# Kernel tuning notes

Measured on AMD Instinct MI355X. Metric: run time of the kernel, lower is better.

The kernel has to match this reference:

```python
import jax, jax.numpy as jnp
import numpy as np

N_TREES = 512
DEPTH = 10
NODES_PER_TREE = 2 ** DEPTH - 1  # 1023, heap-indexed complete binary tree
N = N_TREES * NODES_PER_TREE     # 523776 nodes
X_SIZE = 128
H_SIZE = 128
NUM_CLASSES = 5
VOCAB = 32000


def _level_ids(l):
    """Global node ids for level l (root=0) and their child ids (None for leaves)."""
    start = 2 ** l - 1
    heap = start + np.arange(2 ** l)
    tree_off = np.arange(N_TREES)[:, None] * NODES_PER_TREE
    ids = (tree_off + heap[None, :]).reshape(-1)
    if l < DEPTH - 1:
        child_heap = np.stack([2 * heap + 1, 2 * heap + 2], axis=-1)  # [2^l, 2]
        child = (np.arange(N_TREES)[:, None, None] * NODES_PER_TREE
                 + child_heap[None]).reshape(-1, 2)
        return jnp.asarray(ids), jnp.asarray(child)
    return jnp.asarray(ids), None


def setup_inputs() -> dict:
    key = jax.random.key(0)
    ks = jax.random.split(key, 12)
    s = 0.05
    return {
        "wordid": jax.random.randint(ks[0], (N,), 0, VOCAB),
        "E":      jax.random.normal(ks[1], (VOCAB, X_SIZE), jnp.float32) * s,
        "W_iou":  jax.random.normal(ks[2], (3 * H_SIZE, X_SIZE), jnp.float32) * s,
        "b_iou":  jax.random.normal(ks[3], (3 * H_SIZE,), jnp.float32) * s,
        "U_iou":  jax.random.normal(ks[4], (3 * H_SIZE, H_SIZE), jnp.float32) * s,
        "b_Uiou": jax.random.normal(ks[5], (3 * H_SIZE,), jnp.float32) * s,
        "W_f":    jax.random.normal(ks[6], (H_SIZE, X_SIZE), jnp.float32) * s,
        "b_Wf":   jax.random.normal(ks[7], (H_SIZE,), jnp.float32) * s,
        "U_f":    jax.random.normal(ks[8], (H_SIZE, H_SIZE), jnp.float32) * s,
        "b_Uf":   jax.random.normal(ks[9], (H_SIZE,), jnp.float32) * s,
        "W_out":  jax.random.normal(ks[10], (NUM_CLASSES, H_SIZE), jnp.float32) * s,
        "b_out":  jax.random.normal(ks[11], (NUM_CLASSES,), jnp.float32) * s,
    }


def reference(wordid, E, W_iou, b_iou, U_iou, b_Uiou, W_f, b_Wf, U_f, b_Uf, W_out, b_out):
    mask = (wordid != -1)  # PAD_WORD mask; all-true for generated ids
    x = E[wordid * mask.astype(wordid.dtype)] * mask[:, None].astype(E.dtype)  # [N, X]

    h = jnp.zeros((N, H_SIZE), E.dtype)
    c = jnp.zeros((N, H_SIZE), E.dtype)

    # Topological traversal: leaves (deepest level) up to roots.
    for l in reversed(range(DEPTH)):
        ids, child = _level_ids(l)
        xl = x[ids]  # [M, X]
        if child is None:  # leaves: empty mailbox -> h_tild = c_tild = 0
            h_tild = jnp.zeros((ids.shape[0], H_SIZE), E.dtype)
            c_tild = h_tild
        else:
            hc = h[child]                               # mailbox h: [M, 2, H]
            cc = c[child]                               # mailbox c: [M, 2, H]
            h_tild = hc.sum(axis=1)                     # child-sum
            wx = xl @ W_f.T + b_Wf                      # [M, H]
            uh = hc @ U_f.T + b_Uf                      # [M, 2, H]
            f = jax.nn.sigmoid(wx[:, None, :] + uh)     # per-child forget gate
            c_tild = (f * cc).sum(axis=1)
        iou = xl @ W_iou.T + b_iou + h_tild @ U_iou.T + b_Uiou  # [M, 3H]
        i, o, u = jnp.split(iou, 3, axis=1)
        i, o, u = jax.nn.sigmoid(i), jax.nn.sigmoid(o), jnp.tanh(u)
        cl = i * u + c_tild
        hl = o * jnp.tanh(cl)
        h = h.at[ids].set(hl)
        c = c.at[ids].set(cl)

    # dropout is identity in eval / p=0.0
    logits = h @ W_out.T + b_out  # [N, num_classes]
    return logits
```

## Files before the change

### kernel.cpp

```cpp
#include <hip/hip_runtime.h>

#define H 128
#define TDEPTH 10
#define NPT 1023
#define NTREES 512

typedef unsigned short bf16_t;
typedef unsigned int u32;
typedef __attribute__((ext_vector_type(8))) short bf16x8;
typedef __attribute__((ext_vector_type(4))) float f32x4;

__device__ __forceinline__ float rcp_(float x) { return __builtin_amdgcn_rcpf(x); }
__device__ __forceinline__ float sig_(float x) { return rcp_(1.0f + __expf(-x)); }
__device__ __forceinline__ float th_(float x)  { return 1.0f - 2.0f * rcp_(__expf(2.0f * x) + 1.0f); }
__device__ __forceinline__ float b2f(u32 u) {
    union { float f; u32 u; } v; v.u = u << 16; return v.f;
}
__device__ __forceinline__ bf16_t f2b16(float f) {
    union { float f; u32 u; } v; v.f = f;
    return (bf16_t)((v.u + 0x7fffu + ((v.u >> 16) & 1u)) >> 16);
}
__device__ __forceinline__ bf16x8 ld8(const bf16_t* p) {
    return *reinterpret_cast<const bf16x8*>(p);
}
__device__ __forceinline__ bf16x8 ld8c(const char* p) {
    return *reinterpret_cast<const bf16x8*>(p);
}
__device__ __forceinline__ void gload16(const void* g, void* l) {
    __builtin_amdgcn_global_load_lds(
        (const __attribute__((address_space(1))) void*)g,
        (__attribute__((address_space(3))) void*)l, 16, 0, 0);
}
#define MFMA(a,b,c) __builtin_amdgcn_mfma_f32_16x16x32_bf16(a,b,c,0,0,0)

#define R_H  8192
#define R_C  24576
#define BUFSZ 40960

#define FX_SZ   24576
#define F_H     49152
#define F_C     65536
#define F_LDSSZ 81920

__global__ void pack_weights(const float* __restrict__ W_iou, const float* __restrict__ U_iou,
                             const float* __restrict__ W_f,   const float* __restrict__ U_f,
                             const float* __restrict__ W_out, bf16_t* __restrict__ Wb)
{
    int i = blockIdx.x * 256 + threadIdx.x;
    if (i < 131072) {
        int k    = i & 127;
        int p    = (i >> 7) & 7;
        int feat = i >> 10;
        float v;
        switch (p) {
            case 0: v = W_iou[(      feat) * H + k]; break;
            case 1: v = W_iou[(128 + feat) * H + k]; break;
            case 2: v = W_iou[(256 + feat) * H + k]; break;
            case 3: v = U_iou[(      feat) * H + k]; break;
            case 4: v = U_iou[(128 + feat) * H + k]; break;
            case 5: v = U_iou[(256 + feat) * H + k]; break;
            case 6: v = W_f  [feat * H + k]; break;
            default: v = U_f [feat * H + k]; break;
        }
        Wb[i] = f2b16(v);
    } else {
        int j = i - 131072;
        int cls = j >> 7, k = j & 127;
        Wb[i] = f2b16(cls < 5 ? W_out[cls * H + k] : 0.0f);
    }
}

__global__ void pack_E(const float* __restrict__ E, bf16_t* __restrict__ Eb)
{
    int i = blockIdx.x * 256 + threadIdx.x;
    Eb[i] = f2b16(E[i]);
}

__global__ __launch_bounds__(512, 2) void leaf8_fused(
    const int* __restrict__ wordid, const bf16_t* __restrict__ Eb,
    const bf16_t* __restrict__ Wb,
    const float* __restrict__ b_iou, const float* __restrict__ b_Uiou,
    const float* __restrict__ b_Wf,  const float* __restrict__ b_Uf,
    bf16_t* __restrict__ h_cur, bf16_t* __restrict__ c_cur,
    const float* __restrict__ b_out, float* __restrict__ out,
    int t0, int nt)
{
    extern __shared__ __align__(16) char lds_raw[];

    const int tid  = threadIdx.x;
    const int lane = tid & 63;
    const int w    = tid >> 6;
    const int l15  = lane & 15;
    const int kg   = lane >> 4;
    const int feat = w * 16 + l15;
    const int tilebase = blockIdx.x * nt;

    const float bi  = b_iou[      feat] + b_Uiou[      feat];
    const float bo  = b_iou[128 + feat] + b_Uiou[128 + feat];
    const float bu  = b_iou[256 + feat] + b_Uiou[256 + feat];
    const float bfv = b_Wf[feat] + b_Uf[feat];
    const f32x4 z = {0.f, 0.f, 0.f, 0.f};

    const bf16_t* wbase = Wb + (size_t)feat * 1024 + kg * 8;
    const bf16_t* Wob   = Wb + 131072;

    const int lrow = lane >> 4;
    const int colb = (lane & 15) * 16;

    struct Wids { int a, b, c; };
    auto loadwid = [&](int t) -> Wids {
        Wids r;
        int tb64 = (tilebase + t) * 64, tb32 = (tilebase + t) * 32;
        {   int gl = tb64 + w * 4 + lrow;
            int tt = gl >> 9, ii = gl & 511;
            r.a = wordid[(t0 + tt) * NPT + 511 + ii]; }
        {   int gl = tb64 + 32 + w * 4 + lrow;
            int tt = gl >> 9, ii = gl & 511;
            r.b = wordid[(t0 + tt) * NPT + 511 + ii]; }
        {   int gp = tb32 + w * 4 + lrow;
            int tt = gp >> 8, ii = gp & 255;
            r.c = wordid[(t0 + tt) * NPT + 255 + ii]; }
        return r;
    };

    auto issue = [&](const Wids& wd, char* xbuf) {
        {   int row = w * 4 + lrow;
            gload16((const char*)Eb + (size_t)wd.a * 256 + (colb ^ ((row & 7) << 4)),
                    xbuf + w * 1024); }
        {   int row = 32 + w * 4 + lrow;
            gload16((const char*)Eb + (size_t)wd.b * 256 + (colb ^ ((row & 7) << 4)),
                    xbuf + (w + 8) * 1024); }
        {   int row = w * 4 + lrow;
            gload16((const char*)Eb + (size_t)wd.c * 256 + (colb ^ ((row & 7) << 4)),
                    xbuf + (w + 16) * 1024); }
    };

    Wids wcur = loadwid(0);
    issue(wcur, lds_raw);
    if (nt > 1) wcur = loadwid(1);
    __syncthreads();

    char* h_s = lds_raw + F_H;
    char* c_s = lds_raw + F_C;

    for (int t = 0; t < nt; ++t) {
        char* xbuf  = lds_raw + (t & 1) * FX_SZ;
        char* xleaf = xbuf;
        char* xpar  = xbuf + 16384;
        const int n0 = (tilebase + t) * 32;

        f32x4 lac[3][4];
#pragma unroll
        for (int g = 0; g < 3; ++g)
#pragma unroll
            for (int m = 0; m < 4; ++m) lac[g][m] = z;

#pragma unroll
        for (int ks = 0; ks < 4; ++ks) {
            bf16x8 W0 = ld8(wbase + ks * 32 + 0 * 128);
            bf16x8 W1 = ld8(wbase + ks * 32 + 1 * 128);
            bf16x8 W2 = ld8(wbase + ks * 32 + 2 * 128);
            const int cb = (ks * 32 + kg * 8) * 2;
#pragma unroll
            for (int mt = 0; mt < 4; ++mt) {
                int row = mt * 16 + l15;
                bf16x8 xa = ld8c(xleaf + row * 256 + (cb ^ ((row & 7) << 4)));
                lac[0][mt] = MFMA(xa, W0, lac[0][mt]);
                lac[1][mt] = MFMA(xa, W1, lac[1][mt]);
                lac[2][mt] = MFMA(xa, W2, lac[2][mt]);
            }
        }

        if (t + 1 < nt) {
            issue(wcur, lds_raw + ((t + 1) & 1) * FX_SZ);
            if (t + 2 < nt) wcur = loadwid(t + 2);
        }

#pragma unroll
        for (int mt = 0; mt < 4; ++mt) {
#pragma unroll
            for (int r = 0; r < 4; ++r) {
                int j = mt * 16 + kg * 4 + r;
                float iv = sig_(lac[0][mt][r] + bi);
                float ov = sig_(lac[1][mt][r] + bo);
                float uv = th_ (lac[2][mt][r] + bu);
                float cl = iv * uv;
                float hl = ov * th_(cl);
                int off = j * 256 + ((feat * 2) ^ (((j >> 1) & 7) << 4));
                *(bf16_t*)(h_s + off) = f2b16(hl);
                *(bf16_t*)(c_s + off) = f2b16(cl);
            }
        }
        __syncthreads();

        f32x4 acc[6][2];
#pragma unroll
        for (int g = 0; g < 6; ++g)
#pragma unroll
            for (int m = 0; m < 2; ++m) acc[g][m] = z;

#pragma unroll
        for (int ks = 0; ks < 4; ++ks) {
            bf16x8 W0 = ld8(wbase + ks * 32 + 0 * 128);
            bf16x8 W1 = ld8(wbase + ks * 32 + 1 * 128);
            bf16x8 W2 = ld8(wbase + ks * 32 + 2 * 128);
            bf16x8 W3 = ld8(wbase + ks * 32 + 3 * 128);
            bf16x8 W4 = ld8(wbase + ks * 32 + 4 * 128);
            bf16x8 W5 = ld8(wbase + ks * 32 + 5 * 128);
            bf16x8 W6 = ld8(wbase + ks * 32 + 6 * 128);
            bf16x8 W7 = ld8(wbase + ks * 32 + 7 * 128);
            const int cb = (ks * 32 + kg * 8) * 2;
#pragma unroll
            for (int mt = 0; mt < 2; ++mt) {
                const int row = mt * 16 + l15;
                const int sw  = (row & 7) << 4;
                bf16x8 xa  = ld8c(xpar + row * 256 + (cb ^ sw));
                bf16x8 h0a = ld8c(h_s + (2 * row)     * 256 + (cb ^ sw));
                bf16x8 h1a = ld8c(h_s + (2 * row + 1) * 256 + (cb ^ sw));
                acc[0][mt] = MFMA(h1a, W3, MFMA(h0a, W3, MFMA(xa, W0, acc[0][mt])));
                acc[1][mt] = MFMA(h1a, W4, MFMA(h0a, W4, MFMA(xa, W1, acc[1][mt])));
                acc[2][mt] = MFMA(h1a, W5, MFMA(h0a, W5, MFMA(xa, W2, acc[2][mt])));
                acc[3][mt] = MFMA(xa,  W6, acc[3][mt]);
                acc[4][mt] = MFMA(h0a, W7, acc[4][mt]);
                acc[5][mt] = MFMA(h1a, W7, acc[5][mt]);
            }
        }

        if (w < 4) {
            const int pr = (w & 2) ? 1 : 0;
            const int mbase = (w & 1) * 16;
            f32x4 lacc = z;
#pragma unroll
            for (int ks = 0; ks < 4; ++ks) {
                const int cb = (ks * 32 + kg * 8) * 2;
                int prow = mbase + l15;
                bf16x8 ha = ld8c(h_s + (size_t)(2 * prow + pr) * 256
                                 + (cb ^ ((prow & 7) << 4)));
                bf16x8 wo = ld8(Wob + (size_t)l15 * 128 + ks * 32 + kg * 8);
                lacc = MFMA(ha, wo, lacc);
            }
            if (l15 < 5) {
                float bo5 = b_out[l15];
#pragma unroll
                for (int r = 0; r < 4; ++r) {
                    int m  = mbase + kg * 4 + r;
                    int gc = 2 * (n0 + m) + pr;
                    int tt = gc >> 9, ii = gc & 511;
                    out[(size_t)((t0 + tt) * NPT + 511 + ii) * 5 + l15] = lacc[r] + bo5;
                }
            }
        }

#pragma unroll
        for (int mt = 0; mt < 2; ++mt) {
#pragma unroll
            for (int r = 0; r < 4; ++r) {
                int nb = mt * 16 + kg * 4 + r;
                int g  = n0 + nb;
                float iv = sig_(acc[0][mt][r] + bi);
                float ov = sig_(acc[1][mt][r] + bo);
                float uv = th_ (acc[2][mt][r] + bu);
                float fx = acc[3][mt][r];
                float f0 = sig_(fx + acc[4][mt][r] + bfv);
                float f1 = sig_(fx + acc[5][mt][r] + bfv);
                int co = (feat * 2) ^ ((nb & 7) << 4);
                float c0 = b2f((u32)*(const bf16_t*)(c_s + (2 * nb)     * 256 + co));
                float c1 = b2f((u32)*(const bf16_t*)(c_s + (2 * nb + 1) * 256 + co));
                float cl = iv * uv + f0 * c0 + f1 * c1;
                float hl = ov * th_(cl);
                h_cur[(size_t)g * H + feat] = f2b16(hl);
                c_cur[(size_t)g * H + feat] = f2b16(cl);
            }
        }

        __syncthreads();
    }
}

__global__ __launch_bounds__(512, 2) void internal_mfma(
    const int* __restrict__ wordid, const bf16_t* __restrict__ Eb,
    const bf16_t* __restrict__ Wb,
    const float* __restrict__ b_iou, const float* __restrict__ b_Uiou,
    const float* __restrict__ b_Wf,  const float* __restrict__ b_Uf,
    const bf16_t* __restrict__ h_prev, const bf16_t* __restrict__ c_prev,
    bf16_t* __restrict__ h_cur, bf16_t* __restrict__ c_cur,
    const float* __restrict__ b_out, float* __restrict__ out,
    int level, int t0, int nt)
{
    extern __shared__ __align__(16) char lds_raw[];

    const int tid  = threadIdx.x;
    const int lane = tid & 63;
    const int w    = tid >> 6;
    const int l15  = lane & 15;
    const int kg   = lane >> 4;
    const int feat = w * 16 + l15;
    const int tilebase = blockIdx.x * nt;

    const float bi  = b_iou[      feat] + b_Uiou[      feat];
    const float bo  = b_iou[128 + feat] + b_Uiou[128 + feat];
    const float bu  = b_iou[256 + feat] + b_Uiou[256 + feat];
    const float bfv = b_Wf[feat] + b_Uf[feat];
    const f32x4 z = {0.f, 0.f, 0.f, 0.f};

    const bf16_t* wbase = Wb + (size_t)feat * 1024 + kg * 8;
    const bf16_t* Wob   = Wb + 131072;

    const int lrow = lane >> 4;
    const int colb = (lane & 15) * 16;

    auto issue = [&](int t, char* buf) {
        int n0 = (tilebase + t) * 32;
#pragma unroll
        for (int cc = 0; cc < 5; ++cc) {
            int ch = w + cc * 8;
            const char* src;
            if (ch < 8) {
                int row = ch * 4 + lrow;
                int g = n0 + row;
                int tt = g >> level, ii = g & ((1 << level) - 1);
                int wid = wordid[(t0 + tt) * NPT + (1 << level) - 1 + ii];
                src = (const char*)Eb + (size_t)wid * 256 + (colb ^ ((row & 7) << 4));
            } else if (ch < 24) {
                int row = (ch - 8) * 4 + lrow;
                src = (const char*)h_prev + ((size_t)(2 * n0) + row) * 256
                    + (colb ^ (((row >> 1) & 7) << 4));
            } else {
                int row = (ch - 24) * 4 + lrow;
                src = (const char*)c_prev + ((size_t)(2 * n0) + row) * 256
                    + (colb ^ (((row >> 1) & 7) << 4));
            }
            gload16(src, buf + ch * 1024);
        }
    };

    issue(0, lds_raw);
    __syncthreads();

    for (int t = 0; t < nt; ++t) {
        char* buf = lds_raw + (t & 1) * BUFSZ;
        char* x_s = buf;
        char* h_s = buf + R_H;
        char* c_s = buf + R_C;
        const int n0 = (tilebase + t) * 32;

        f32x4 acc[6][2];
#pragma unroll
        for (int g = 0; g < 6; ++g)
#pragma unroll
            for (int m = 0; m < 2; ++m) acc[g][m] = z;

#pragma unroll
        for (int ks = 0; ks < 4; ++ks) {
            const int cb = (ks * 32 + kg * 8) * 2;
            bf16x8 W0 = ld8(wbase + ks * 32 + 0 * 128);
            bf16x8 W1 = ld8(wbase + ks * 32 + 1 * 128);
            bf16x8 W2 = ld8(wbase + ks * 32 + 2 * 128);
            bf16x8 W3 = ld8(wbase + ks * 32 + 3 * 128);
            bf16x8 W4 = ld8(wbase + ks * 32 + 4 * 128);
            bf16x8 W5 = ld8(wbase + ks * 32 + 5 * 128);
            bf16x8 W6 = ld8(wbase + ks * 32 + 6 * 128);
            bf16x8 W7 = ld8(wbase + ks * 32 + 7 * 128);
#pragma unroll
            for (int mt = 0; mt < 2; ++mt) {
                const int row = mt * 16 + l15;
                const int sw  = (row & 7) << 4;
                bf16x8 xa  = ld8c(x_s + row * 256 + (cb ^ sw));
                bf16x8 h0a = ld8c(h_s + (2 * row)     * 256 + (cb ^ sw));
                bf16x8 h1a = ld8c(h_s + (2 * row + 1) * 256 + (cb ^ sw));
                acc[0][mt] = MFMA(h1a, W3, MFMA(h0a, W3, MFMA(xa, W0, acc[0][mt])));
                acc[1][mt] = MFMA(h1a, W4, MFMA(h0a, W4, MFMA(xa, W1, acc[1][mt])));
                acc[2][mt] = MFMA(h1a, W5, MFMA(h0a, W5, MFMA(xa, W2, acc[2][mt])));
                acc[3][mt] = MFMA(xa,  W6, acc[3][mt]);
                acc[4][mt] = MFMA(h0a, W7, acc[4][mt]);
                acc[5][mt] = MFMA(h1a, W7, acc[5][mt]);
            }
        }

        if (t + 1 < nt) issue(t + 1, lds_raw + ((t + 1) & 1) * BUFSZ);

        if (w < 4) {
            const int pr = (w & 2) ? 1 : 0;
            const int mbase = (w & 1) * 16;
            f32x4 lacc = z;
#pragma unroll
            for (int ks = 0; ks < 4; ++ks) {
                const int cb = (ks * 32 + kg * 8) * 2;
                int prow = mbase + l15;
                bf16x8 ha = ld8c(h_s + (size_t)(2 * prow + pr) * 256
                                 + (cb ^ ((prow & 7) << 4)));
                bf16x8 wo = ld8(Wob + (size_t)l15 * 128 + ks * 32 + kg * 8);
                lacc = MFMA(ha, wo, lacc);
            }
            if (l15 < 5) {
                float bo5 = b_out[l15];
                int lc = level + 1;
#pragma unroll
                for (int r = 0; r < 4; ++r) {
                    int m  = mbase + kg * 4 + r;
                    int gc = 2 * (n0 + m) + pr;
                    int tt = gc >> lc, ii = gc & ((1 << lc) - 1);
                    out[(size_t)((t0 + tt) * NPT + (1 << lc) - 1 + ii) * 5 + l15] = lacc[r] + bo5;
                }
            }
        }

#pragma unroll
        for (int mt = 0; mt < 2; ++mt) {
#pragma unroll
            for (int r = 0; r < 4; ++r) {
                int nb = mt * 16 + kg * 4 + r;
                int g  = n0 + nb;
                float iv = sig_(acc[0][mt][r] + bi);
                float ov = sig_(acc[1][mt][r] + bo);
                float uv = th_ (acc[2][mt][r] + bu);
                float fx = acc[3][mt][r];
                float f0 = sig_(fx + acc[4][mt][r] + bfv);
                float f1 = sig_(fx + acc[5][mt][r] + bfv);
                int co = (feat * 2) ^ ((nb & 7) << 4);
                float c0 = b2f((u32)*(const bf16_t*)(c_s + (2 * nb)     * 256 + co));
                float c1 = b2f((u32)*(const bf16_t*)(c_s + (2 * nb + 1) * 256 + co));
                float cl = iv * uv + f0 * c0 + f1 * c1;
                float hl = ov * th_(cl);
                h_cur[(size_t)g * H + feat] = f2b16(hl);
                c_cur[(size_t)g * H + feat] = f2b16(cl);
            }
        }

        __syncthreads();
    }
}

__global__ void logits_root(
    const bf16_t* __restrict__ h0buf, const float* __restrict__ W_out,
    const float* __restrict__ b_out, float* __restrict__ out,
    int M, int t0)
{
    int wv     = (blockIdx.x * blockDim.x + threadIdx.x) >> 6;
    int lane   = threadIdx.x & 63;
    int nwaves = (gridDim.x * blockDim.x) >> 6;
    for (int g = wv; g < M; g += nwaves) {
        float h0 = b2f((u32)h0buf[(size_t)g * H + lane]);
        float h1 = b2f((u32)h0buf[(size_t)g * H + 64 + lane]);
#pragma unroll
        for (int c = 0; c < 5; ++c) {
            float p = h0 * W_out[c * H + lane] + h1 * W_out[c * H + 64 + lane];
#pragma unroll
            for (int off = 32; off >= 1; off >>= 1) p += __shfl_xor(p, off, 64);
            if (lane == 0) out[(size_t)(t0 + g) * NPT * 5 + c] = p + b_out[c];
        }
    }
}

extern "C" void kernel_launch(void* const* d_in, const int* in_sizes, int n_in,
                              void* d_out, int out_size, void* d_ws, size_t ws_size,
                              hipStream_t stream)
{
    (void)in_sizes; (void)n_in; (void)out_size;
    const int*   wordid = (const int*)  d_in[0];
    const float* E      = (const float*)d_in[1];
    const float* W_iou  = (const float*)d_in[2];
    const float* b_iou  = (const float*)d_in[3];
    const float* U_iou  = (const float*)d_in[4];
    const float* b_Uiou = (const float*)d_in[5];
    const float* W_f    = (const float*)d_in[6];
    const float* b_Wf   = (const float*)d_in[7];
    const float* U_f    = (const float*)d_in[8];
    const float* b_Uf   = (const float*)d_in[9];
    const float* W_out  = (const float*)d_in[10];
    const float* b_out  = (const float*)d_in[11];
    float* out = (float*)d_out;

    bf16_t* Wb = (bf16_t*)d_ws;
    bf16_t* Eb = Wb + 133120;
    bf16_t* dyn = Eb + (size_t)32000 * H;
    const size_t fixed_bytes = (133120 + (size_t)32000 * H) * 2;

    int C = 1;
    while (C < 16 && fixed_bytes + (size_t)(NTREES / C) * 262144u > ws_size) C <<= 1;
    const int T = NTREES / C;

    bf16_t* hA = dyn;
    bf16_t* cA = hA + (size_t)T * 256 * H;
    bf16_t* hB = cA + (size_t)T * 256 * H;
    bf16_t* cB = hB + (size_t)T * 256 * H;

    pack_weights<<<520, 256, 0, stream>>>(W_iou, U_iou, W_f, U_f, W_out, Wb);
    pack_E<<<16000, 256, 0, stream>>>(E, Eb);

    for (int chunk = 0; chunk < C; ++chunk) {
        int t0 = chunk * T;

        {
            int tiles  = (T << 8) / 32;
            int blocks = tiles < 256 ? tiles : 256;
            int nt     = tiles / blocks;
            leaf8_fused<<<blocks, 512, F_LDSSZ, stream>>>(
                wordid, Eb, Wb, b_iou, b_Uiou, b_Wf, b_Uf,
                hB, cB, b_out, out, t0, nt);
        }

        for (int l = TDEPTH - 3; l >= 0; --l) {
            int M = T << l;
            bf16_t* h_cur  = (l & 1) ? hA : hB;
            bf16_t* c_cur  = (l & 1) ? cA : cB;
            bf16_t* h_prev = (l & 1) ? hB : hA;
            bf16_t* c_prev = (l & 1) ? cB : cA;

            int tiles  = M / 32;
            int blocks = tiles < 256 ? tiles : 256;
            if (blocks < 1) blocks = 1;
            int nt     = tiles / blocks;
            internal_mfma<<<blocks, 512, 2 * BUFSZ, stream>>>(
                wordid, Eb, Wb, b_iou, b_Uiou, b_Wf, b_Uf,
                h_prev, c_prev, h_cur, c_cur, b_out, out, l, t0, nt);
        }
        int blocksR = (T / 4 < 4096) ? ((T + 3) / 4) : 4096;
        if (blocksR < 1) blocksR = 1;
        logits_root<<<blocksR, 256, 0, stream>>>(hB, W_out, b_out, out, T, t0);
    }
}
```

Before: 319.8 us.

## Fuse pairs of internal tree levels into one kernel via LDS-resident intermediates

Replaces the per-level internal kernel with a pair_fused kernel that computes two consecutive tree levels per launch. The lower level's h/c results for a 64-node supertile stay in LDS and feed the parent level directly, so that level's global write and re-read disappear and the number of launches drops. In exchange, LDS use per block grows to about 120KB, each tile adds extra barriers, and prefetch overlap is limited to the two mid-level buffers, which may reduce occupancy and parallelism at the upper levels.

```diff
diff --git a/kernel.cpp b/kernel.cpp
--- a/kernel.cpp
+++ b/kernel.cpp
@@ -33,14 +33,17 @@
 }
 #define MFMA(a,b,c) __builtin_amdgcn_mfma_f32_16x16x32_bf16(a,b,c,0,0,0)
 
-#define R_H  8192
-#define R_C  24576
-#define BUFSZ 40960
-
 #define FX_SZ   24576
 #define F_H     49152
 #define F_C     65536
 #define F_LDSSZ 81920
+
+#define P_BUF0  0
+#define P_BUF1  40960
+#define P_RH    81920
+#define P_RC    98304
+#define P_XP    114688
+#define P_LDSSZ 122880
 
 __global__ void pack_weights(const float* __restrict__ W_iou, const float* __restrict__ U_iou,
                              const float* __restrict__ W_f,   const float* __restrict__ U_f,
@@ -277,15 +280,15 @@
     }
 }
 
-__global__ __launch_bounds__(512, 2) void internal_mfma(
+__global__ __launch_bounds__(512, 2) void pair_fused(
     const int* __restrict__ wordid, const bf16_t* __restrict__ Eb,
     const bf16_t* __restrict__ Wb,
     const float* __restrict__ b_iou, const float* __restrict__ b_Uiou,
     const float* __restrict__ b_Wf,  const float* __restrict__ b_Uf,
-    const bf16_t* __restrict__ h_prev, const bf16_t* __restrict__ c_prev,
-    bf16_t* __restrict__ h_cur, bf16_t* __restrict__ c_cur,
+    const bf16_t* __restrict__ h_gp, const bf16_t* __restrict__ c_gp,
+    bf16_t* __restrict__ h_out, bf16_t* __restrict__ c_out,
     const float* __restrict__ b_out, float* __restrict__ out,
-    int level, int t0, int nt)
+    int lm, int t0, int nt)
 {
     extern __shared__ __align__(16) char lds_raw[];
 
@@ -296,6 +299,7 @@
     const int kg   = lane >> 4;
     const int feat = w * 16 + l15;
     const int tilebase = blockIdx.x * nt;
+    const int lp = lm - 1, lg = lm + 1;
 
     const float bi  = b_iou[      feat] + b_Uiou[      feat];
     const float bo  = b_iou[128 + feat] + b_Uiou[128 + feat];
@@ -309,46 +313,49 @@
     const int lrow = lane >> 4;
     const int colb = (lane & 15) * 16;
 
-    auto issue = [&](int t, char* buf) {
-        int n0 = (tilebase + t) * 32;
+    auto issue_mid = [&](int n0m, char* buf) {
 #pragma unroll
         for (int cc = 0; cc < 5; ++cc) {
             int ch = w + cc * 8;
             const char* src;
             if (ch < 8) {
                 int row = ch * 4 + lrow;
-                int g = n0 + row;
-                int tt = g >> level, ii = g & ((1 << level) - 1);
-                int wid = wordid[(t0 + tt) * NPT + (1 << level) - 1 + ii];
+                int g = n0m + row;
+                int tt = g >> lm, ii = g & ((1 << lm) - 1);
+                int wid = wordid[(t0 + tt) * NPT + (1 << lm) - 1 + ii];
                 src = (const char*)Eb + (size_t)wid * 256 + (colb ^ ((row & 7) << 4));
             } else if (ch < 24) {
                 int row = (ch - 8) * 4 + lrow;
-                src = (const char*)h_prev + ((size_t)(2 * n0) + row) * 256
+                src = (const char*)h_gp + ((size_t)(2 * n0m) + row) * 256
                     + (colb ^ (((row >> 1) & 7) << 4));
             } else {
                 int row = (ch - 24) * 4 + lrow;
-                src = (const char*)c_prev + ((size_t)(2 * n0) + row) * 256
+                src = (const char*)c_gp + ((size_t)(2 * n0m) + row) * 256
                     + (colb ^ (((row >> 1) & 7) << 4));
             }
             gload16(src, buf + ch * 1024);
         }
     };
-
-    issue(0, lds_raw);
-    __syncthreads();
-
-    for (int t = 0; t < nt; ++t) {
-        char* buf = lds_raw + (t & 1) * BUFSZ;
+    auto issue_xp = [&](int st) {
+        int row = w * 4 + lrow;
+        int g = st * 32 + row;
+        int tt = g >> lp, ii = g & ((1 << lp) - 1);
+        int wid = wordid[(t0 + tt) * NPT + (1 << lp) - 1 + ii];
+        gload16((const char*)Eb + (size_t)wid * 256 + (colb ^ ((row & 7) << 4)),
+                lds_raw + P_XP + w * 1024);
+    };
+
+    auto mid_phase = [&](int st, int m, char* buf) {
+        const int n0m = st * 64 + m * 32;
         char* x_s = buf;
-        char* h_s = buf + R_H;
-        char* c_s = buf + R_C;
-        const int n0 = (tilebase + t) * 32;
+        char* h_s = buf + 8192;
+        char* c_s = buf + 24576;
 
         f32x4 acc[6][2];
 #pragma unroll
         for (int g = 0; g < 6; ++g)
 #pragma unroll
-            for (int m = 0; m < 2; ++m) acc[g][m] = z;
+            for (int mt = 0; mt < 2; ++mt) acc[g][mt] = z;
 
 #pragma unroll
         for (int ks = 0; ks < 4; ++ks) {
@@ -377,8 +384,6 @@
             }
         }
 
-        if (t + 1 < nt) issue(t + 1, lds_raw + ((t + 1) & 1) * BUFSZ);
-
         if (w < 4) {
             const int pr = (w & 2) ? 1 : 0;
             const int mbase = (w & 1) * 16;
@@ -394,13 +399,12 @@
             }
             if (l15 < 5) {
                 float bo5 = b_out[l15];
-                int lc = level + 1;
 #pragma unroll
                 for (int r = 0; r < 4; ++r) {
-                    int m  = mbase + kg * 4 + r;
-                    int gc = 2 * (n0 + m) + pr;
-                    int tt = gc >> lc, ii = gc & ((1 << lc) - 1);
-                    out[(size_t)((t0 + tt) * NPT + (1 << lc) - 1 + ii) * 5 + l15] = lacc[r] + bo5;
+                    int mm = mbase + kg * 4 + r;
+                    int gc = 2 * (n0m + mm) + pr;
+                    int tt = gc >> lg, ii = gc & ((1 << lg) - 1);
+                    out[(size_t)((t0 + tt) * NPT + (1 << lg) - 1 + ii) * 5 + l15] = lacc[r] + bo5;
                 }
             }
         }
@@ -410,7 +414,6 @@
 #pragma unroll
             for (int r = 0; r < 4; ++r) {
                 int nb = mt * 16 + kg * 4 + r;
-                int g  = n0 + nb;
                 float iv = sig_(acc[0][mt][r] + bi);
                 float ov = sig_(acc[1][mt][r] + bo);
                 float uv = th_ (acc[2][mt][r] + bu);
@@ -422,11 +425,115 @@
                 float c1 = b2f((u32)*(const bf16_t*)(c_s + (2 * nb + 1) * 256 + co));
                 float cl = iv * uv + f0 * c0 + f1 * c1;
                 float hl = ov * th_(cl);
-                h_cur[(size_t)g * H + feat] = f2b16(hl);
-                c_cur[(size_t)g * H + feat] = f2b16(cl);
-            }
-        }
-
+                int off = (m * 32 + nb) * 256 + ((feat * 2) ^ (((nb >> 1) & 7) << 4));
+                *(bf16_t*)(lds_raw + P_RH + off) = f2b16(hl);
+                *(bf16_t*)(lds_raw + P_RC + off) = f2b16(cl);
+            }
+        }
+    };
+
+    issue_mid(tilebase * 64,      lds_raw + P_BUF0);
+    issue_mid(tilebase * 64 + 32, lds_raw + P_BUF1);
+    issue_xp(tilebase);
+    __syncthreads();
+
+    for (int t = 0; t < nt; ++t) {
+        const int st = tilebase + t;
+        if (t > 0) issue_xp(st);
+
+        mid_phase(st, 0, lds_raw + P_BUF0);
+        __syncthreads();
+        if (t + 1 < nt) issue_mid((st + 1) * 64, lds_raw + P_BUF0);
+
+        mid_phase(st, 1, lds_raw + P_BUF1);
+        __syncthreads();
+        if (t + 1 < nt) issue_mid((st + 1) * 64 + 32, lds_raw + P_BUF1);
+
+        {
+            char* xp = lds_raw + P_XP;
+            char* rh = lds_raw + P_RH;
+            char* rc = lds_raw + P_RC;
+
+            f32x4 acc[6][2];
+#pragma unroll
+            for (int g = 0; g < 6; ++g)
+#pragma unroll
+                for (int mt = 0; mt < 2; ++mt) acc[g][mt] = z;
+
+#pragma unroll
+            for (int ks = 0; ks < 4; ++ks) {
+                const int cb = (ks * 32 + kg * 8) * 2;
+                bf16x8 W0 = ld8(wbase + ks * 32 + 0 * 128);
+                bf16x8 W1 = ld8(wbase + ks * 32 + 1 * 128);
+                bf16x8 W2 = ld8(wbase + ks * 32 + 2 * 128);
+                bf16x8 W3 = ld8(wbase + ks * 32 + 3 * 128);
+                bf16x8 W4 = ld8(wbase + ks * 32 + 4 * 128);
+                bf16x8 W5 = ld8(wbase + ks * 32 + 5 * 128);
+                bf16x8 W6 = ld8(wbase + ks * 32 + 6 * 128);
+                bf16x8 W7 = ld8(wbase + ks * 32 + 7 * 128);
+#pragma unroll
+                for (int mt = 0; mt < 2; ++mt) {
+                    const int row = mt * 16 + l15;
+                    const int sw  = (row & 7) << 4;
+                    bf16x8 xa  = ld8c(xp + row * 256 + (cb ^ sw));
+                    bf16x8 h0a = ld8c(rh + (2 * row)     * 256 + (cb ^ sw));
+                    bf16x8 h1a = ld8c(rh + (2 * row + 1) * 256 + (cb ^ sw));
+                    acc[0][mt] = MFMA(h1a, W3, MFMA(h0a, W3, MFMA(xa, W0, acc[0][mt])));
+                    acc[1][mt] = MFMA(h1a, W4, MFMA(h0a, W4, MFMA(xa, W1, acc[1][mt])));
+                    acc[2][mt] = MFMA(h1a, W5, MFMA(h0a, W5, MFMA(xa, W2, acc[2][mt])));
+                    acc[3][mt] = MFMA(xa,  W6, acc[3][mt]);
+                    acc[4][mt] = MFMA(h0a, W7, acc[4][mt]);
+                    acc[5][mt] = MFMA(h1a, W7, acc[5][mt]);
+                }
+            }
+
+            if (w < 4) {
+                const int pr = (w & 2) ? 1 : 0;
+                const int mbase = (w & 1) * 16;
+                f32x4 lacc = z;
+#pragma unroll
+                for (int ks = 0; ks < 4; ++ks) {
+                    const int cb = (ks * 32 + kg * 8) * 2;
+                    int prow = mbase + l15;
+                    bf16x8 ha = ld8c(rh + (size_t)(2 * prow + pr) * 256
+                                     + (cb ^ ((prow & 7) << 4)));
+                    bf16x8 wo = ld8(Wob + (size_t)l15 * 128 + ks * 32 + kg * 8);
+                    lacc = MFMA(ha, wo, lacc);
+                }
+                if (l15 < 5) {
+                    float bo5 = b_out[l15];
+#pragma unroll
+                    for (int r = 0; r < 4; ++r) {
+                        int mm = mbase + kg * 4 + r;
+                        int gc = 2 * (st * 32 + mm) + pr;
+                        int tt = gc >> lm, ii = gc & ((1 << lm) - 1);
+                        out[(size_t)((t0 + tt) * NPT + (1 << lm) - 1 + ii) * 5 + l15] = lacc[r] + bo5;
+                    }
+                }
+            }
+
+#pragma unroll
+            for (int mt = 0; mt < 2; ++mt) {
+#pragma unroll
+                for (int r = 0; r < 4; ++r) {
+                    int nb = mt * 16 + kg * 4 + r;
+                    int p  = st * 32 + nb;
+                    float iv = sig_(acc[0][mt][r] + bi);
+                    float ov = sig_(acc[1][mt][r] + bo);
+                    float uv = th_ (acc[2][mt][r] + bu);
+                    float fx = acc[3][mt][r];
+                    float f0 = sig_(fx + acc[4][mt][r] + bfv);
+                    float f1 = sig_(fx + acc[5][mt][r] + bfv);
+                    int co = (feat * 2) ^ ((nb & 7) << 4);
+                    float c0 = b2f((u32)*(const bf16_t*)(rc + (2 * nb)     * 256 + co));
+                    float c1 = b2f((u32)*(const bf16_t*)(rc + (2 * nb + 1) * 256 + co));
+                    float cl = iv * uv + f0 * c0 + f1 * c1;
+                    float hl = ov * th_(cl);
+                    h_out[(size_t)p * H + feat] = f2b16(hl);
+                    c_out[(size_t)p * H + feat] = f2b16(cl);
+                }
+            }
+        }
         __syncthreads();
     }
 }
@@ -500,23 +607,23 @@
                 hB, cB, b_out, out, t0, nt);
         }
 
-        for (int l = TDEPTH - 3; l >= 0; --l) {
-            int M = T << l;
-            bf16_t* h_cur  = (l & 1) ? hA : hB;
-            bf16_t* c_cur  = (l & 1) ? cA : cB;
-            bf16_t* h_prev = (l & 1) ? hB : hA;
-            bf16_t* c_prev = (l & 1) ? cB : cA;
-
-            int tiles  = M / 32;
-            int blocks = tiles < 256 ? tiles : 256;
+        const bf16_t* hin = hB; const bf16_t* cin = cB;
+        bf16_t* hout = hA;      bf16_t* cout = cA;
+        for (int lm = 7; lm >= 1; lm -= 2) {
+            int sts    = (T << (lm - 1)) / 32;
+            int blocks = sts < 256 ? sts : 256;
             if (blocks < 1) blocks = 1;
-            int nt     = tiles / blocks;
-            internal_mfma<<<blocks, 512, 2 * BUFSZ, stream>>>(
+            int nt     = sts / blocks;
+            pair_fused<<<blocks, 512, P_LDSSZ, stream>>>(
                 wordid, Eb, Wb, b_iou, b_Uiou, b_Wf, b_Uf,
-                h_prev, c_prev, h_cur, c_cur, b_out, out, l, t0, nt);
-        }
+                hin, cin, hout, cout, b_out, out, lm, t0, nt);
+            const bf16_t* th = hin; const bf16_t* tc = cin;
+            hin = hout; cin = cout;
+            hout = (bf16_t*)th; cout = (bf16_t*)tc;
+        }
+
         int blocksR = (T / 4 < 4096) ? ((T + 3) / 4) : 4096;
         if (blocksR < 1) blocksR = 1;
-        logits_root<<<blocksR, 256, 0, stream>>>(hB, W_out, b_out, out, T, t0);
+        logits_root<<<blocksR, 256, 0, stream>>>(hin, W_out, b_out, out, T, t0);
     }
 }
```

New measurement: 322.7 us. About the same (+0.9%).
